# Optimization experiments

Measured on AMD Instinct MI355X. Metric: run time of the kernel, lower is better.

Reference implementation:

```python
import jax, jax.numpy as jnp
import numpy as np

B, S, D = 32, 512, 768
DSYM, DROLE = 32, 32
H = DSYM * DROLE  # LSTM hidden = out_dim = dSymbols*dRoles
NSYM, NROLE = 50, 35
TEMP = 1.0


def setup_inputs() -> dict:
    key = jax.random.key(0)
    ks = jax.random.split(key, 12)
    n = lambda k, shp, s=0.02: jax.random.normal(k, shp, dtype=jnp.float32) * s
    return {
        "x": jax.random.normal(ks[0], (B, S, D), dtype=jnp.float32),
        "WihF": n(ks[1], (4 * H, D)), "WhhF": n(ks[2], (4 * H, H)),
        "bihF": jnp.zeros((4 * H,), jnp.float32), "bhhF": jnp.zeros((4 * H,), jnp.float32),
        "WihR": n(ks[3], (4 * H, D)), "WhhR": n(ks[4], (4 * H, H)),
        "bihR": jnp.zeros((4 * H,), jnp.float32), "bhhR": jnp.zeros((4 * H,), jnp.float32),
        "WaF_w": n(ks[5], (NSYM, H)), "WaF_b": jnp.zeros((NSYM,), jnp.float32),
        "WaR_w": n(ks[6], (NROLE, H)), "WaR_b": jnp.zeros((NROLE,), jnp.float32),
        "F_w": n(ks[7], (DSYM, NSYM)), "R_w": n(ks[8], (DROLE, NROLE)),
        "scale_F": jnp.float32(1.0), "scale_R": jnp.float32(1.0),
    }


def _lstm_cell(x_t, h, c, Wih, Whh, bih, bhh):
    # PyTorch LSTM gate order: i, f, g, o
    g = x_t @ Wih.T + bih + h @ Whh.T + bhh  # [B, 4H]
    i, f, gg, o = jnp.split(g, 4, axis=-1)
    c = jax.nn.sigmoid(f) * c + jax.nn.sigmoid(i) * jnp.tanh(gg)
    h = jax.nn.sigmoid(o) * jnp.tanh(c)
    return h, c


def reference(x, WihF, WhhF, bihF, bhhF, WihR, WhhR, bihR, bhhR,
              WaF_w, WaF_b, WaR_w, WaR_b, F_w, R_w, scale_F, scale_R):
    batch = x.shape[0]

    def step(carry, x_t):
        T, cF, cR = carry  # hidden h of BOTH cells is overwritten by TPR binding T
        hF, cF = _lstm_cell(x_t, T, cF, WihF, WhhF, bihF, bhhF)
        hR, cR = _lstm_cell(x_t, T, cR, WihR, WhhR, bihR, bhhR)
        aF = jax.nn.softmax((hF @ WaF_w.T + WaF_b) / TEMP, axis=-1)  # [B, NSYM]
        aR = jax.nn.softmax((hR @ WaR_w.T + WaR_b) / TEMP, axis=-1)  # [B, NROLE]
        itemF = scale_F * (aF @ F_w.T)  # [B, DSYM]  (ScaleLinear, no bias)
        itemR = scale_R * (aR @ R_w.T)  # [B, DROLE]
        Tn = jnp.einsum('bs,br->bsr', itemF, itemR).reshape(batch, H)
        return (Tn, cF, cR), (Tn, aF, aR)

    z = jnp.zeros((batch, H), x.dtype)
    _, (outs, aFs, aRs) = jax.lax.scan(step, (z, z, z), jnp.swapaxes(x, 0, 1))
    # back to batch-first: out [B,S,H], aFs [B,S,NSYM], aRs [B,S,NROLE]
    return (jnp.swapaxes(outs, 0, 1), jnp.swapaxes(aFs, 0, 1), jnp.swapaxes(aRs, 0, 1))
```

## Files before the change

kernel.cpp:

```cpp
#include <hip/hip_runtime.h>
#include <stdint.h>
#include <stddef.h>

#define B_   32
#define S_   512
#define D_   768
#define H_   1024
#define NF_  50
#define NR_  35
#define NRP_ 36
#define NWG  256
#define WGS  256

#define ITB_OFF   32768
#define PF_OFF    65536
#define XBF_OFF   1703936
#define PF_F_SZ   102400
#define PF_STEP   176128

typedef __attribute__((ext_vector_type(8))) short sh8;
typedef __attribute__((ext_vector_type(4))) float f4;
typedef __attribute__((ext_vector_type(2))) float f2v;
typedef __attribute__((ext_vector_type(4))) unsigned int u4x;
typedef unsigned long long u64;

__device__ __forceinline__ unsigned short f2bf(float f) {
  unsigned int u = __float_as_uint(f);
  u += 0x7fffu + ((u >> 16) & 1u);
  return (unsigned short)(u >> 16);
}

__device__ __forceinline__ unsigned cvtpk_bf16(float lo, float hi) {
  unsigned r;
  asm("v_cvt_pk_bf16_f32 %0, %1, %2" : "=v"(r) : "v"(lo), "v"(hi));
  return r;
}

__device__ __forceinline__ sh8 cvt8(const float* __restrict__ p) {
  f4 av = *(const f4*)p;
  f4 bv = *(const f4*)(p + 4);
  union { sh8 s; unsigned short us[8]; } r;
  r.us[0] = f2bf(av[0]); r.us[1] = f2bf(av[1]); r.us[2] = f2bf(av[2]); r.us[3] = f2bf(av[3]);
  r.us[4] = f2bf(bv[0]); r.us[5] = f2bf(bv[1]); r.us[6] = f2bf(bv[2]); r.us[7] = f2bf(bv[3]);
  return r.s;
}

__device__ __forceinline__ float sigm(float x) { return 1.f / (1.f + __expf(-x)); }

__device__ __forceinline__ float tanhfast(float x) {
  const float e = __expf(2.f * x);
  return 1.f - 2.f / (e + 1.f);
}

__device__ __forceinline__ u64 pack2(float a, float b) {
  return (u64)__float_as_uint(a) | ((u64)__float_as_uint(b) << 32);
}

__device__ __forceinline__ u64 tagv(float v, unsigned t) {
  return (u64)__float_as_uint(v) | ((u64)t << 32);
}
__device__ __forceinline__ float    valof(u64 p) { return __uint_as_float((unsigned)p); }
__device__ __forceinline__ unsigned tagof(u64 p) { return (unsigned)(p >> 32); }

template<int NA, int NPAIR>
__device__ __forceinline__ void pf_store(int tid, int wIdx, int b0,
                                         const float* __restrict__ h_lds,
                                         const float* __restrict__ Wa_l,
                                         u64* __restrict__ d64) {
  const int tot = 16 * NPAIR;
  for (int i = tid; i < tot; i += WGS) {
    const int bl = i / NPAIR, k = i - bl * NPAIR;
    const int n0 = 2 * k, n1 = 2 * k + 1;
    float v0 = 0.f, v1 = 0.f;
    #pragma unroll
    for (int jj = 0; jj < 16; ++jj) v0 += h_lds[bl * 16 + jj] * Wa_l[n0 * 17 + jj];
    if (n1 < NA) {
      #pragma unroll
      for (int jj = 0; jj < 16; ++jj) v1 += h_lds[bl * 16 + jj] * Wa_l[n1 * 17 + jj];
    }
    __hip_atomic_store(&d64[(size_t)((b0 + bl) * 64 + wIdx) * NPAIR + k], pack2(v0, v1),
                       __ATOMIC_RELAXED, __HIP_MEMORY_SCOPE_AGENT);
  }
}

template<int NAR, int NAPR>
__device__ __forceinline__ void reduce_tail(
    int tid, int wave, int lane,
    const u64* __restrict__ src64, float* __restrict__ stage,
    float (* __restrict__ red4)[64], float* __restrict__ arow,
    const float* __restrict__ bA, const float* __restrict__ WL, float sc,
    u64* __restrict__ itRowT, unsigned stag,
    float* __restrict__ outRow)
{
  u64* st64 = (u64*)stage;
  constexpr int n64 = (64 * NAPR) >> 1;
  for (int i = tid; i < n64; i += WGS)
    st64[i] = __hip_atomic_load(&src64[i], __ATOMIC_RELAXED, __HIP_MEMORY_SCOPE_AGENT);
  __syncthreads();
  {
    const int n = (lane < NAR) ? lane : 0;
    float v = 0.f;
    #pragma unroll
    for (int w2 = 0; w2 < 16; ++w2) v += stage[(wave * 16 + w2) * NAPR + n];
    red4[wave][lane] = v;
  }
  __syncthreads();
  if (wave == 0) {
    const int n = (lane < NAR) ? lane : 0;
    const float v = red4[0][lane] + red4[1][lane] + red4[2][lane] + red4[3][lane];
    float e = (lane < NAR) ? __expf(v + bA[n]) : 0.f;
    float ssum = e;
    #pragma unroll
    for (int off = 1; off < 64; off <<= 1) ssum += __shfl_xor(ssum, off, 64);
    const float a = e / ssum;
    if (lane < NAR) arow[lane] = a;
    {
      constexpr int KH = (NAR + 1) >> 1;
      const int dr = lane & 31;
      float it = 0.f;
      if (lane < 32) {
        #pragma unroll
        for (int k = 0; k < KH; ++k) it += arow[k] * WL[dr * NAR + k];
      } else {
        #pragma unroll
        for (int k = KH; k < NAR; ++k) it += arow[k] * WL[dr * NAR + k];
      }
      it += __shfl_xor(it, 32, 64);
      if (lane < 32)
        __hip_atomic_store(&itRowT[lane], tagv(it * sc, stag),
                           __ATOMIC_RELAXED, __HIP_MEMORY_SCOPE_AGENT);
    }
    if (lane < NAR) outRow[lane] = a;
  }
}

__global__ void init_ws(unsigned int* __restrict__ flags) {
  const int t = blockIdx.x * blockDim.x + threadIdx.x;
  const int stride = gridDim.x * blockDim.x;
  for (int i = t; i < 16384; i += stride)
    __hip_atomic_store(&flags[i], 0u, __ATOMIC_RELAXED, __HIP_MEMORY_SCOPE_AGENT);
}

__global__ void xcvt(const float* __restrict__ x, unsigned int* __restrict__ xb2, int ndw) {
  const int stride = gridDim.x * blockDim.x;
  for (int o = blockIdx.x * blockDim.x + threadIdx.x; o < ndw; o += stride) {
    const int e2  = o & 3;
    const int l   = (o >> 2) & 63;
    const int tb  = o >> 8;
    const int t   = tb % 24;
    const int bts = tb / 24;
    const int bt  = bts & 1;
    const int s   = bts >> 1;
    const int b   = bt * 16 + (l & 15);
    const int k   = t * 32 + (l >> 4) * 8 + e2 * 2;
    const f2v v = ((const f2v*)x)[(((size_t)b * S_ + s) * D_ + k) >> 1];
    xb2[o] = (unsigned int)f2bf(v[0]) | ((unsigned int)f2bf(v[1]) << 16);
  }
}

__global__ __launch_bounds__(WGS, 1) void tpr_persist(
    const float* __restrict__ x, const unsigned short* __restrict__ xbf, int xmode,
    const float* __restrict__ WihF, const float* __restrict__ WhhF,
    const float* __restrict__ bihF, const float* __restrict__ bhhF,
    const float* __restrict__ WihR, const float* __restrict__ WhhR,
    const float* __restrict__ bihR, const float* __restrict__ bhhR,
    const float* __restrict__ WaFw, const float* __restrict__ WaFb,
    const float* __restrict__ WaRw, const float* __restrict__ WaRb,
    const float* __restrict__ Fw, const float* __restrict__ Rw,
    const float* __restrict__ scFp, const float* __restrict__ scRp,
    float* __restrict__ out0, unsigned char* __restrict__ ws)
{
  __shared__ __align__(16) float part[4][16 * 69];
  __shared__ float h_lds[16 * 16];
  __shared__ __align__(16) float itF_l[16 * 36];
  __shared__ __align__(16) float itR_l[16 * 36];
  __shared__ float Fw_l[32 * NF_];
  __shared__ float Rw_l[32 * NR_];
  __shared__ float Wa_l[NF_ * 17];
  __shared__ float red4[4][64];
  __shared__ float arow[64];
  __shared__ float bias_l[64];
  __shared__ float bF_l[NF_];
  __shared__ float bR_l[NR_];

  const int wg    = blockIdx.x;
  const int tid   = threadIdx.x;
  const int wave  = tid >> 6;
  const int lane  = tid & 63;
  const int n16   = lane & 15;
  const int quad  = lane >> 4;
  const int group = wg >> 6;
  const bool isF  = wg < 128;
  const int hb    = group & 1;
  const int b0    = hb * 16;
  const int wIdx  = wg & 63;
  const int j0    = wIdx * 16;
  const int gbase = group << 6;
  const float* Wih = isF ? WihF : WihR;
  const float* Whh = isF ? WhhF : WhhR;
  const float* bih = isF ? bihF : bihR;
  const float* bhh = isF ? bhhF : bhhR;
  const float* Wa  = isF ? WaFw : WaRw;
  const int NA  = isF ? NF_ : NR_;

  unsigned int* wtag = (unsigned int*)ws;
  u64* itb = (u64*)(ws + ITB_OFF);
  float* pf    = (float*)(ws + PF_OFF);

  sh8 whhf[4][8];
  sh8 wihf[4][6];
  #pragma unroll
  for (int g = 0; g < 4; ++g) {
    const int row = g * 1024 + j0 + n16;
    #pragma unroll
    for (int ks = 0; ks < 8; ++ks)
      whhf[g][ks] = cvt8(Whh + (size_t)row * H_ + wave * 256 + ks * 32 + quad * 8);
    #pragma unroll
    for (int ks = 0; ks < 6; ++ks)
      wihf[g][ks] = cvt8(Wih + (size_t)row * D_ + wave * 192 + ks * 32 + quad * 8);
  }

  if (tid < 64) {
    const int row = (tid >> 4) * 1024 + j0 + (tid & 15);
    bias_l[tid] = bih[row] + bhh[row];
  }
  for (int i = tid; i < NA * 16; i += WGS)
    Wa_l[(i >> 4) * 17 + (i & 15)] = Wa[(size_t)(i >> 4) * H_ + j0 + (i & 15)];
  for (int i = tid; i < 32 * NF_; i += WGS) Fw_l[i] = Fw[i];
  for (int i = tid; i < 32 * NR_; i += WGS) Rw_l[i] = Rw[i];
  if (tid < NF_) bF_l[tid] = WaFb[tid];
  if (tid < NR_) bR_l[tid] = WaRb[tid];
  const float sF = scFp[0];
  const float sR = scRp[0];
  float cc = 0.f;

  f4 xacc[4];
  const f4 fz = {0.f, 0.f, 0.f, 0.f};

  auto xpart = [&](int sx) {
    #pragma unroll
    for (int g = 0; g < 4; ++g) xacc[g] = fz;
    #pragma unroll
    for (int ks = 0; ks < 6; ++ks) {
      sh8 xa;
      if (xmode == 0) {
        const size_t toff = ((size_t)((sx * 2 + hb) * 24 + wave * 6 + ks) << 9)
                            + (size_t)lane * 8;
        union { u4x u; sh8 s; } t;
        t.u = *(const u4x*)(xbf + toff);
        xa = t.s;
      } else {
        const size_t off = ((size_t)(b0 + n16) * S_ + sx) * D_ + wave * 192 + ks * 32 + quad * 8;
        xa = cvt8(x + off);
      }
      #pragma unroll
      for (int g = 0; g < 4; ++g)
        xacc[g] = __builtin_amdgcn_mfma_f32_16x16x32_bf16(xa, wihf[g][ks], xacc[g], 0, 0, 0);
    }
  };

  xpart(0);
  __syncthreads();

  float* out1 = out0 + (size_t)B_ * S_ * H_;
  float* out2 = out1 + (size_t)B_ * S_ * NF_;

  const bool isRed = (wIdx < 16);
  const int  redB  = b0 + wIdx;
  const bool redF  = isF;
  const int  redJ  = (redF ? 0 : 32) + redB;

  for (int s = 0; s < S_; ++s) {
    const int buf = s & 1;
    const unsigned int stag = (unsigned int)(s + 1);

    f4 acc[4];
    #pragma unroll
    for (int g = 0; g < 4; ++g) acc[g] = xacc[g];
    if (s > 0) {
      const f4 fA0 = *(const f4*)&itF_l[n16 * 36 + (wave << 3)];
      const f4 fA1 = *(const f4*)&itF_l[n16 * 36 + (wave << 3) + 4];
      const f4 rA0 = *(const f4*)&itR_l[n16 * 36 + (quad << 3)];
      const f4 rA1 = *(const f4*)&itR_l[n16 * 36 + (quad << 3) + 4];
      #pragma unroll
      for (int ks = 0; ks < 8; ++ks) {
        const float fs = (ks < 4) ? fA0[ks & 3] : fA1[ks & 3];
        union { sh8 s8; u4x u; } t;
        t.u[0] = cvtpk_bf16(fs * rA0[0], fs * rA0[1]);
        t.u[1] = cvtpk_bf16(fs * rA0[2], fs * rA0[3]);
        t.u[2] = cvtpk_bf16(fs * rA1[0], fs * rA1[1]);
        t.u[3] = cvtpk_bf16(fs * rA1[2], fs * rA1[3]);
        #pragma unroll
        for (int g = 0; g < 4; ++g)
          acc[g] = __builtin_amdgcn_mfma_f32_16x16x32_bf16(t.s8, whhf[g][ks], acc[g], 0, 0, 0);
      }
    }
    #pragma unroll
    for (int g = 0; g < 4; ++g)
      #pragma unroll
      for (int r = 0; r < 4; ++r)
        part[wave][(quad * 4 + r) * 69 + g * 16 + n16] = acc[g][r];
    __syncthreads();

    {
      const int bl = tid >> 4;
      const int jj = tid & 15;
      float G[4];
      #pragma unroll
      for (int g = 0; g < 4; ++g) {
        const int n = g * 16 + jj;
        G[g] = bias_l[n] + part[0][bl * 69 + n] + part[1][bl * 69 + n]
                         + part[2][bl * 69 + n] + part[3][bl * 69 + n];
      }
      const float ig = sigm(G[0]);
      const float fg = sigm(G[1]);
      const float gg = tanhfast(G[2]);
      const float og = sigm(G[3]);
      cc = fg * cc + ig * gg;
      h_lds[bl * 16 + jj] = og * tanhfast(cc);
    }
    __syncthreads();

    if (isF)
      pf_store<NF_, (NF_ >> 1)>(tid, wIdx, b0, h_lds, Wa_l,
          (u64*)(pf + (size_t)buf * PF_STEP));
    else
      pf_store<NR_, (NRP_ >> 1)>(tid, wIdx, b0, h_lds, Wa_l,
          (u64*)(pf + (size_t)buf * PF_STEP + PF_F_SZ));
    __syncthreads();
    if (tid == 0)
      __hip_atomic_store(&wtag[wg * 32], stag, __ATOMIC_RELAXED, __HIP_MEMORY_SCOPE_AGENT);

    if (isRed) {
      if (wave == 0) {
        for (;;) {
          const unsigned int v = __hip_atomic_load(&wtag[(gbase + lane) * 32],
                                                   __ATOMIC_RELAXED, __HIP_MEMORY_SCOPE_AGENT);
          if (__ballot(v >= stag) == ~0ull) break;
          __builtin_amdgcn_s_sleep(1);
        }
      }
      __syncthreads();
      if (redF)
        reduce_tail<NF_, NF_>(tid, wave, lane,
            (const u64*)(pf + (size_t)buf * PF_STEP + (size_t)redB * 64 * NF_),
            &part[0][0], red4, arow, bF_l, Fw_l, sF,
            &itb[((size_t)buf * 64 + redJ) * 32], stag,
            &out1[((size_t)redB * S_ + s) * NF_]);
      else
        reduce_tail<NR_, NRP_>(tid, wave, lane,
            (const u64*)(pf + (size_t)buf * PF_STEP + PF_F_SZ + (size_t)redB * 64 * NRP_),
            &part[0][0], red4, arow, bR_l, Rw_l, sR,
            &itb[((size_t)buf * 64 + redJ) * 32], stag,
            &out2[((size_t)redB * S_ + s) * NR_]);
    }

    if (s + 1 < S_) xpart(s + 1);

    {
      const u64* src = itb + (size_t)buf * 64 * 32;
      float vals[4];
      unsigned sm = 0;
      #pragma unroll
      for (int k2 = 0; k2 < 4; ++k2) {
        const int i = tid + k2 * WGS;
        const int lr = i >> 5, col = i & 31;
        const int grow = (lr < 16) ? (b0 + lr) : (32 + b0 + (lr - 16));
        const u64 p = __hip_atomic_load(&src[(size_t)grow * 32 + col],
                                        __ATOMIC_RELAXED, __HIP_MEMORY_SCOPE_AGENT);
        vals[k2] = valof(p);
        sm |= (tagof(p) != stag) ? (1u << k2) : 0u;
      }
      while (sm) {
        __builtin_amdgcn_s_sleep(1);
        #pragma unroll
        for (int k2 = 0; k2 < 4; ++k2) if (sm & (1u << k2)) {
          const int i = tid + k2 * WGS;
          const int lr = i >> 5, col = i & 31;
          const int grow = (lr < 16) ? (b0 + lr) : (32 + b0 + (lr - 16));
          const u64 p = __hip_atomic_load(&src[(size_t)grow * 32 + col],
                                          __ATOMIC_RELAXED, __HIP_MEMORY_SCOPE_AGENT);
          if (tagof(p) == stag) { vals[k2] = valof(p); sm &= ~(1u << k2); }
        }
      }
      #pragma unroll
      for (int k2 = 0; k2 < 4; ++k2) {
        const int i = tid + k2 * WGS;
        const int lr = i >> 5, col = i & 31;
        if (lr < 16) itF_l[lr * 36 + col] = vals[k2];
        else         itR_l[(lr - 16) * 36 + col] = vals[k2];
      }
    }
    __syncthreads();

    if (isF && wIdx >= 32 && wIdx < 48) {
      const int bl = wIdx - 32;
      const int ds = tid >> 3, dr0 = (tid & 7) * 4;
      f4 v;
      #pragma unroll
      for (int q = 0; q < 4; ++q) v[q] = itF_l[bl * 36 + ds] * itR_l[bl * 36 + dr0 + q];
      *(f4*)&out0[((size_t)(b0 + bl) * S_ + s) * H_ + tid * 4] = v;
    }
  }
}

extern "C" void kernel_launch(void* const* d_in, const int* in_sizes, int n_in,
                              void* d_out, int out_size, void* d_ws, size_t ws_size,
                              hipStream_t stream) {
  (void)in_sizes; (void)n_in; (void)out_size;
  const float* x    = (const float*)d_in[0];
  const float* WihF = (const float*)d_in[1];
  const float* WhhF = (const float*)d_in[2];
  const float* bihF = (const float*)d_in[3];
  const float* bhhF = (const float*)d_in[4];
  const float* WihR = (const float*)d_in[5];
  const float* WhhR = (const float*)d_in[6];
  const float* bihR = (const float*)d_in[7];
  const float* bihR2= (const float*)d_in[8];
  const float* WaFw = (const float*)d_in[9];
  const float* WaFb = (const float*)d_in[10];
  const float* WaRw = (const float*)d_in[11];
  const float* WaRb = (const float*)d_in[12];
  const float* Fw   = (const float*)d_in[13];
  const float* Rw   = (const float*)d_in[14];
  const float* scF  = (const float*)d_in[15];
  const float* scR  = (const float*)d_in[16];

  unsigned char* ws = (unsigned char*)d_ws;
  unsigned short* xbf = (unsigned short*)(ws + XBF_OFF);
  const size_t need = (size_t)XBF_OFF + (size_t)B_ * S_ * D_ * 2;
  const int xmode = (ws_size >= need) ? 0 : 1;

  init_ws<<<8, 256, 0, stream>>>((unsigned int*)ws);
  if (xmode == 0)
    xcvt<<<2048, 256, 0, stream>>>(x, (unsigned int*)xbf, (B_ * S_ * D_) / 2);
  tpr_persist<<<NWG, WGS, 0, stream>>>(x, xbf, xmode,
      WihF, WhhF, bihF, bhhF, WihR, WhhR, bihR, bihR2,
      WaFw, WaFb, WaRw, WaRb, Fw, Rw, scF, scR,
      (float*)d_out, ws);
}
```

Measured before the change: 4.333 ms.

## Replace workgroup barriers with per-wave flag signaling in the reduction handoff

Each wave now waits for its own global stores and bumps an LDS counter, and the last wave to arrive publishes the workgroup's step tag, so the barrier before the tag store is gone. In the reducer, each wave polls only the 16 producer tags whose partials it will stage and loads just its own slice, which removes a barrier and the single-wave poll. The first back-off sleep on the itb poll is also made longer. This trades block-wide barriers for finer-grained waits, but relies on relaxed atomics and an s_waitcnt for ordering with no explicit release fence, so cross-CU visibility is a risk.

```diff
diff --git a/kernel.cpp b/kernel.cpp
--- a/kernel.cpp
+++ b/kernel.cpp
@@ -86,17 +86,27 @@
 template<int NAR, int NAPR>
 __device__ __forceinline__ void reduce_tail(
     int tid, int wave, int lane,
+    const unsigned int* __restrict__ wtagG, unsigned stag,
     const u64* __restrict__ src64, float* __restrict__ stage,
     float (* __restrict__ red4)[64], float* __restrict__ arow,
     const float* __restrict__ bA, const float* __restrict__ WL, float sc,
-    u64* __restrict__ itRowT, unsigned stag,
+    u64* __restrict__ itRowT,
     float* __restrict__ outRow)
 {
+  {
+    const int w = wave * 16 + (lane & 15);
+    for (;;) {
+      const unsigned int v = __hip_atomic_load(&wtagG[w * 32],
+                                               __ATOMIC_RELAXED, __HIP_MEMORY_SCOPE_AGENT);
+      if (__ballot(v >= stag) == ~0ull) break;
+      __builtin_amdgcn_s_sleep(1);
+    }
+  }
   u64* st64 = (u64*)stage;
-  constexpr int n64 = (64 * NAPR) >> 1;
-  for (int i = tid; i < n64; i += WGS)
-    st64[i] = __hip_atomic_load(&src64[i], __ATOMIC_RELAXED, __HIP_MEMORY_SCOPE_AGENT);
-  __syncthreads();
+  constexpr int n64w = (16 * NAPR) >> 1;
+  for (int i = lane; i < n64w; i += 64)
+    st64[wave * n64w + i] = __hip_atomic_load(&src64[wave * n64w + i],
+                                              __ATOMIC_RELAXED, __HIP_MEMORY_SCOPE_AGENT);
   {
     const int n = (lane < NAR) ? lane : 0;
     float v = 0.f;
@@ -182,6 +192,7 @@
   __shared__ float bias_l[64];
   __shared__ float bF_l[NF_];
   __shared__ float bR_l[NR_];
+  __shared__ unsigned int dsCnt;
 
   const int wg    = blockIdx.x;
   const int tid   = threadIdx.x;
@@ -220,6 +231,7 @@
       wihf[g][ks] = cvt8(Wih + (size_t)row * D_ + wave * 192 + ks * 32 + quad * 8);
   }
 
+  if (tid == 0) dsCnt = 0u;
   if (tid < 64) {
     const int row = (tid >> 4) * 1024 + j0 + (tid & 15);
     bias_l[tid] = bih[row] + bhh[row];
@@ -327,31 +339,28 @@
     else
       pf_store<NR_, (NRP_ >> 1)>(tid, wIdx, b0, h_lds, Wa_l,
           (u64*)(pf + (size_t)buf * PF_STEP + PF_F_SZ));
-    __syncthreads();
-    if (tid == 0)
-      __hip_atomic_store(&wtag[wg * 32], stag, __ATOMIC_RELAXED, __HIP_MEMORY_SCOPE_AGENT);
+    __asm__ __volatile__("s_waitcnt vmcnt(0)" ::: "memory");
+    if (lane == 0) {
+      const unsigned int old = __hip_atomic_fetch_add(&dsCnt, 1u,
+                                    __ATOMIC_RELAXED, __HIP_MEMORY_SCOPE_WORKGROUP);
+      if (old == 4u * stag - 1u)
+        __hip_atomic_store(&wtag[wg * 32], stag, __ATOMIC_RELAXED, __HIP_MEMORY_SCOPE_AGENT);
+    }
 
     if (isRed) {
-      if (wave == 0) {
-        for (;;) {
-          const unsigned int v = __hip_atomic_load(&wtag[(gbase + lane) * 32],
-                                                   __ATOMIC_RELAXED, __HIP_MEMORY_SCOPE_AGENT);
-          if (__ballot(v >= stag) == ~0ull) break;
-          __builtin_amdgcn_s_sleep(1);
-        }
-      }
-      __syncthreads();
       if (redF)
         reduce_tail<NF_, NF_>(tid, wave, lane,
+            &wtag[gbase * 32], stag,
             (const u64*)(pf + (size_t)buf * PF_STEP + (size_t)redB * 64 * NF_),
             &part[0][0], red4, arow, bF_l, Fw_l, sF,
-            &itb[((size_t)buf * 64 + redJ) * 32], stag,
+            &itb[((size_t)buf * 64 + redJ) * 32],
             &out1[((size_t)redB * S_ + s) * NF_]);
       else
         reduce_tail<NR_, NRP_>(tid, wave, lane,
+            &wtag[gbase * 32], stag,
             (const u64*)(pf + (size_t)buf * PF_STEP + PF_F_SZ + (size_t)redB * 64 * NRP_),
             &part[0][0], red4, arow, bR_l, Rw_l, sR,
-            &itb[((size_t)buf * 64 + redJ) * 32], stag,
+            &itb[((size_t)buf * 64 + redJ) * 32],
             &out2[((size_t)redB * S_ + s) * NR_]);
     }
 
@@ -371,8 +380,10 @@
         vals[k2] = valof(p);
         sm |= (tagof(p) != stag) ? (1u << k2) : 0u;
       }
+      bool first = true;
       while (sm) {
-        __builtin_amdgcn_s_sleep(1);
+        if (first) { __builtin_amdgcn_s_sleep(4); first = false; }
+        else       { __builtin_amdgcn_s_sleep(1); }
         #pragma unroll
         for (int k2 = 0; k2 < 4; ++k2) if (sm & (1u << k2)) {
           const int i = tid + k2 * WGS;
```

Result: slower. 4.617 ms (+6.5%).
